# Kernel optimization log

Measured on AMD Instinct MI355X. Metric: run time of the kernel, lower is better.

The kernel has to match this reference:

```python
import jax, jax.numpy as jnp
import numpy as np
import math

D_MODEL = 1024
FFN = 4096
NUM_HEAD = 16
HEAD_DIM = 64
BATCH = 4
SEQ = 2048
EPS = 1e-5


def _lin(k, out_dim, in_dim):
    bound = 1.0 / math.sqrt(in_dim)
    k1, k2 = jax.random.split(k)
    W = jax.random.uniform(k1, (out_dim, in_dim), jnp.float32, -bound, bound)
    b = jax.random.uniform(k2, (out_dim,), jnp.float32, -bound, bound)
    return W, b


def setup_inputs() -> dict:
    key = jax.random.key(0)
    ks = jax.random.split(key, 12)
    x = jax.random.normal(ks[0], (BATCH, SEQ, D_MODEL), jnp.float32)
    mask = jnp.zeros((SEQ, SEQ), jnp.float32)  # additive mask, broadcast over [H,B,S,S]
    Wq, bq = _lin(ks[1], D_MODEL, D_MODEL)
    Wk, bk = _lin(ks[2], D_MODEL, D_MODEL)
    Wv, bv = _lin(ks[3], D_MODEL, D_MODEL)
    Wo, bo = _lin(ks[4], D_MODEL, D_MODEL)
    gamma = jnp.ones((D_MODEL,), jnp.float32)
    beta = jnp.zeros((D_MODEL,), jnp.float32)
    W1, b1 = _lin(ks[5], FFN, D_MODEL)
    W2, b2 = _lin(ks[6], FFN // 2, FFN)
    W3, b3 = _lin(ks[7], FFN // 4, FFN // 2)
    W4, b4 = _lin(ks[8], D_MODEL, FFN // 4)
    Wl, bl = _lin(ks[9], D_MODEL, D_MODEL)
    return dict(x=x, mask=mask, Wq=Wq, bq=bq, Wk=Wk, bk=bk, Wv=Wv, bv=bv,
                Wo=Wo, bo=bo, gamma=gamma, beta=beta,
                W1=W1, b1=b1, W2=W2, b2=b2, W3=W3, b3=b3, W4=W4, b4=b4,
                Wl=Wl, bl=bl)


def _layernorm(x, gamma, beta):
    mean = jnp.mean(x, axis=-1, keepdims=True)
    var = jnp.mean((x - mean) ** 2, axis=-1, keepdims=True)
    return gamma * ((x - mean) / jnp.sqrt(var + EPS)) + beta


def _attention(x, mask, Wq, bq, Wk, bk, Wv, bv, Wo, bo):
    B, S, _ = x.shape
    def heads(W, b):
        return (x @ W.T + b).reshape(B, S, NUM_HEAD, HEAD_DIM).transpose(0, 2, 1, 3)
    q, k, v = heads(Wq, bq), heads(Wk, bk), heads(Wv, bv)  # [B,H,S,D]
    scaled = jnp.einsum('bhsd,bhtd->bhst', q, k) / math.sqrt(HEAD_DIM)
    # faithful to source: permute to [H,B,S,S], add mask, softmax, NaN->0,
    # then sum over dim=1 (which is BATCH here) -> [H,S,S]
    scaled = scaled.transpose(1, 0, 2, 3) + mask
    attn = jax.nn.softmax(scaled, axis=-1)
    attn = jnp.where(jnp.isnan(attn), 0.0, attn)
    A = jnp.sum(attn, axis=1)  # [H,S,S]
    V = jnp.einsum('hst,bhtd->bhsd', A, v)  # broadcast matmul as in torch
    V = V.transpose(0, 2, 1, 3).reshape(B, S, NUM_HEAD * HEAD_DIM)
    return V @ Wo.T + bo


def _ffn(x, W1, b1, W2, b2, W3, b3, W4, b4):
    x = jax.nn.relu(x @ W1.T + b1)
    x = jax.nn.relu(x @ W2.T + b2)
    x = jax.nn.relu(x @ W3.T + b3)
    return x @ W4.T + b4


def reference(x, mask, Wq, bq, Wk, bk, Wv, bv, Wo, bo, gamma, beta,
              W1, b1, W2, b2, W3, b3, W4, b4, Wl, bl):
    res = x
    x = _attention(x, mask, Wq, bq, Wk, bk, Wv, bv, Wo, bo)
    x = _layernorm(x + res, gamma, beta)
    res = x
    x = _ffn(x, W1, b1, W2, b2, W3, b3, W4, b4)
    x = _layernorm(res + x, gamma, beta)
    return x @ Wl.T + bl
```

## Files before the change

### kernel.cpp

```cpp
#include <hip/hip_runtime.h>
#include <stdint.h>

#define SEQL 2048
#define DM 1024
#define NH 16
#define DHD 64
#define NB 4
#define MT 8192

typedef __attribute__((ext_vector_type(8))) short bf16x8;
typedef __attribute__((ext_vector_type(4))) float f32x4;

__device__ __forceinline__ unsigned short f2bf(float f) {
  uint32_t u = __builtin_bit_cast(uint32_t, f);
  return (unsigned short)((u + 0x7FFFu + ((u >> 16) & 1u)) >> 16);
}
__device__ __forceinline__ float bf2f(unsigned short h) {
  return __builtin_bit_cast(float, (uint32_t)h << 16);
}
__device__ __forceinline__ float fexp2(float x) {
  float r;
  asm volatile("v_exp_f32 %0, %1" : "=v"(r) : "v"(x));
  return r;
}
__device__ __forceinline__ void glds16(const void* g, void* l) {
  __builtin_amdgcn_global_load_lds(
      (const __attribute__((address_space(1))) void*)g,
      (__attribute__((address_space(3))) void*)l, 16, 0, 0);
}
__device__ __forceinline__ void bar() {
  asm volatile("" ::: "memory");
  __builtin_amdgcn_s_barrier();
  asm volatile("" ::: "memory");
}
__device__ __forceinline__ void vm4() { asm volatile("s_waitcnt vmcnt(4)" ::: "memory"); }
__device__ __forceinline__ void vm0() { asm volatile("s_waitcnt vmcnt(0)" ::: "memory"); }

__global__ __launch_bounds__(256) void cast_f32_bf16(
    const float* __restrict__ in, unsigned short* __restrict__ out, int n8) {
  int i = blockIdx.x * 256 + threadIdx.x;
  if (i >= n8) return;
  const float4* p = (const float4*)(in + (size_t)i * 8);
  float4 a = p[0], b = p[1];
  uint32_t w0 = f2bf(a.x) | ((uint32_t)f2bf(a.y) << 16);
  uint32_t w1 = f2bf(a.z) | ((uint32_t)f2bf(a.w) << 16);
  uint32_t w2 = f2bf(b.x) | ((uint32_t)f2bf(b.y) << 16);
  uint32_t w3 = f2bf(b.z) | ((uint32_t)f2bf(b.w) << 16);
  int4 v = {(int)w0, (int)w1, (int)w2, (int)w3};
  *(int4*)(out + (size_t)i * 8) = v;
}

__global__ __launch_bounds__(256) void addb(
    const unsigned short* __restrict__ a, unsigned short* __restrict__ bio, int n8) {
  int i = blockIdx.x * 256 + threadIdx.x;
  if (i >= n8) return;
  int4 va = *(const int4*)(a + (size_t)i * 8);
  int4 vb = *(const int4*)(bio + (size_t)i * 8);
  uint32_t* pa = (uint32_t*)&va;
  uint32_t* pb = (uint32_t*)&vb;
  int4 vo;
  uint32_t* po = (uint32_t*)&vo;
#pragma unroll
  for (int j = 0; j < 4; j++) {
    float lo = bf2f((unsigned short)pa[j]) + bf2f((unsigned short)pb[j]);
    float hi = bf2f((unsigned short)(pa[j] >> 16)) + bf2f((unsigned short)(pb[j] >> 16));
    po[j] = f2bf(lo) | ((uint32_t)f2bf(hi) << 16);
  }
  *(int4*)(bio + (size_t)i * 8) = vo;
}

__global__ __launch_bounds__(256) void vtrans(
    const unsigned short* __restrict__ V, unsigned short* __restrict__ Vt) {
  __shared__ unsigned short td[64][72];
  const int blk = blockIdx.x;
  const int t64 = blk & 31;
  const int b = (blk >> 5) & 3;
  const int h = blk >> 7;
  const int tid = threadIdx.x;
  const int r = tid >> 3, c8 = (tid & 7) * 8;
  const unsigned short* src = V + (size_t)(b * SEQL + t64 * 64) * DM + h * 64;
#pragma unroll
  for (int half = 0; half < 2; half++) {
    int4 v = *(const int4*)(src + (size_t)(r + half * 32) * DM + c8);
    *(int4*)&td[r + half * 32][c8] = v;
  }
  __syncthreads();
  unsigned short* dst = Vt + (size_t)((h * 4 + b) * 64) * SEQL + t64 * 64;
#pragma unroll
  for (int half = 0; half < 2; half++) {
    int tk = tid + half * 256;
    int d = tk >> 3, tc = (tk & 7) * 8;
    unsigned short tmp[8];
#pragma unroll
    for (int j = 0; j < 8; j++) tmp[j] = td[tc + j][d];
    *(int4*)(dst + (size_t)d * SEQL + tc) = *(int4*)tmp;
  }
}

template <int MS, int NS, int MR, int MH>
__device__ __forceinline__ void mmaQ(f32x4 (&acc)[MR][4],
                                     const bf16x8 (&Ar)[MH][2],
                                     const bf16x8 (&Br)[2][2]) {
  __builtin_amdgcn_s_setprio(1);
#pragma unroll
  for (int m = 0; m < MH; m++)
#pragma unroll
    for (int n = 0; n < 2; n++)
#pragma unroll
      for (int kk = 0; kk < 2; kk++)
        acc[MS * MH + m][NS * 2 + n] = __builtin_amdgcn_mfma_f32_16x16x32_bf16(
            Ar[m][kk], Br[n][kk], acc[MS * MH + m][NS * 2 + n], 0, 0, 0);
  __builtin_amdgcn_s_setprio(0);
}

template <int MH>
__device__ __forceinline__ void loadF(bf16x8 (&Ar)[MH][2], const char* base,
                                      int row0, int g) {
#pragma unroll
  for (int m = 0; m < MH; m++) {
    int row = row0 + m * 16;
    int sw = (row & 7) << 4;
    Ar[m][0] = *(const bf16x8*)(base + row * 128 + ((g << 4) ^ sw));
    Ar[m][1] = *(const bf16x8*)(base + row * 128 + (((4 + g) << 4) ^ sw));
  }
}

template <int BM, bool RELU, int OMODE>
__global__ __launch_bounds__(512, 2) void gemm8(
    const unsigned short* __restrict__ Ag, const unsigned short* __restrict__ Bg,
    const float* __restrict__ bias0, const float* __restrict__ bias1,
    const float* __restrict__ bias2, void* C0, void* C1, void* C2, int N, int K,
    float sc0) {
  constexpr int MR = BM / 32;
  constexpr int MH = MR / 2;
  constexpr int AT = BM * 128;
  constexpr int BT = 256 * 128;
  __shared__ __align__(16) char lds[2 * AT + 2 * BT];
  char* Ab0 = lds;
  char* Ab1 = lds + AT;
  char* Bb0 = lds + 2 * AT;
  char* Bb1 = lds + 2 * AT + BT;

  const int tid = threadIdx.x;
  const int wid = tid >> 6, lane = tid & 63;
  const int wr = wid >> 2, wc = wid & 3;
  const int g = lane >> 4, ln = lane & 15;

  const int nbx = N >> 8;
  const int nwg = gridDim.x;
  const int cpx = nwg >> 3;
  const int wg = (blockIdx.x & 7) * cpx + (blockIdx.x >> 3);
  const int bm = wg / nbx, bn = wg % nbx;

  f32x4 acc[MR][4];
#pragma unroll
  for (int m = 0; m < MR; m++)
#pragma unroll
    for (int n = 0; n < 4; n++) acc[m][n] = (f32x4){0.f, 0.f, 0.f, 0.f};

  const int srow = wid * 8 + (lane >> 3);
  const int cs8 = ((lane & 7) ^ (lane >> 3)) * 8;
  const unsigned short* aBase = Ag + (size_t)(bm * BM + srow) * K + cs8;
  const unsigned short* bBase = Bg + (size_t)(bn * 256 + srow) * K + cs8;
  const int wofs = wid * 1024;

  auto stageA = [&](char* buf, int tt, int h) {
    const unsigned short* src = aBase + (size_t)(h * (BM / 2)) * K + tt * 64;
    char* dst = buf + h * (AT / 2) + wofs;
    glds16(src, dst);
    if constexpr (BM == 256) glds16(src + (size_t)64 * K, dst + 8192);
  };
  auto stageB = [&](char* buf, int tt, int h) {
    const unsigned short* src = bBase + (size_t)(h * 128) * K + tt * 64;
    char* dst = buf + h * (BT / 2) + wofs;
    glds16(src, dst);
    glds16(src + (size_t)64 * K, dst + 8192);
  };

  const int np = K >> 7;
  const int rowA0 = wr * (BM / 2) + ln;
  const int rowB0 = wc * 64 + ln;

  stageA(Ab0, 0, 0);
  stageA(Ab0, 0, 1);
  stageB(Bb0, 0, 0);
  stageB(Bb0, 0, 1);
  stageB(Bb1, 1, 0);
  stageB(Bb1, 1, 1);
  vm4();
  bar();

  bf16x8 Ar[MH][2], Br0[2][2], Br1[2][2];
  for (int i = 0; i < np; i++) {
    const int t = 2 * i;
    const bool sg = (i + 1 < np);
    loadF<MH>(Ar, Ab0, rowA0, g);
    loadF<2>(Br0, Bb0, rowB0, g);
    stageA(Ab1, t + 1, 0);
    bar();
    mmaQ<0, 0>(acc, Ar, Br0);
    bar();
    loadF<2>(Br1, Bb0, rowB0 + 32, g);
    stageA(Ab1, t + 1, 1);
    bar();
    mmaQ<0, 1>(acc, Ar, Br1);
    bar();
    loadF<MH>(Ar, Ab0, rowA0 + MH * 16, g);
    if (sg) stageB(Bb0, t + 2, 0);
    bar();
    mmaQ<1, 1>(acc, Ar, Br1);
    bar();
    if (sg) stageB(Bb0, t + 2, 1);
    bar();
    mmaQ<1, 0>(acc, Ar, Br0);
    if (sg) vm4(); else vm0();
    bar();
    loadF<MH>(Ar, Ab1, rowA0, g);
    loadF<2>(Br0, Bb1, rowB0, g);
    if (sg) stageA(Ab0, t + 2, 0);
    bar();
    mmaQ<0, 0>(acc, Ar, Br0);
    bar();
    loadF<2>(Br1, Bb1, rowB0 + 32, g);
    if (sg) stageA(Ab0, t + 2, 1);
    bar();
    mmaQ<0, 1>(acc, Ar, Br1);
    bar();
    loadF<MH>(Ar, Ab1, rowA0 + MH * 16, g);
    if (sg) stageB(Bb1, t + 3, 0);
    bar();
    mmaQ<1, 1>(acc, Ar, Br1);
    bar();
    if (sg) stageB(Bb1, t + 3, 1);
    bar();
    mmaQ<1, 0>(acc, Ar, Br0);
    if (sg) vm4();
    bar();
  }

  const int c0 = bn * 256 + wc * 64;
  const float* bias = bias0;
  float scl = sc0;
  unsigned short* outb = (unsigned short*)C0;
  float* outf = (float*)C0;
  int ldC = N;
  if constexpr (OMODE == 2) {
    int seg = bn >> 2;
    bias = seg == 0 ? bias0 : (seg == 1 ? bias1 : bias2);
    outb = (unsigned short*)(seg == 0 ? C0 : (seg == 1 ? C1 : C2));
    scl = seg == 0 ? sc0 : 1.0f;
    ldC = 1024;
  }
#pragma unroll
  for (int am = 0; am < MR; am++) {
#pragma unroll
    for (int n = 0; n < 4; n++) {
      int col = c0 + n * 16 + ln;
      int colL = (OMODE == 2) ? (col & 1023) : col;
      float bv = bias[colL];
#pragma unroll
      for (int r = 0; r < 4; r++) {
        int row = bm * BM + wr * (BM / 2) + am * 16 + g * 4 + r;
        float v = (acc[am][n][r] + bv) * scl;
        if constexpr (RELU) v = fmaxf(v, 0.f);
        if constexpr (OMODE == 0)
          outf[(size_t)row * ldC + colL] = v;
        else
          outb[(size_t)row * ldC + colL] = f2bf(v);
      }
    }
  }
}

__global__ __launch_bounds__(256) void attn_stats(
    const unsigned short* __restrict__ Q, const unsigned short* __restrict__ Kb,
    float* __restrict__ lst) {
  __shared__ unsigned short sK[64 * 64];
  const int blk = blockIdx.x;
  const int sblk = blk & 31;
  const int bh = blk >> 5;
  const int b = bh >> 4, h = bh & 15;
  const int tid = threadIdx.x;
  const int wid = tid >> 6, lane = tid & 63;
  const int g = lane >> 4;
  const int s0 = sblk * 64 + wid * 16;

  const unsigned short* qp =
      Q + (size_t)(b * SEQL + s0 + (lane & 15)) * DM + h * DHD + g * 8;
  bf16x8 q0 = *(const bf16x8*)qp;
  bf16x8 q1 = *(const bf16x8*)(qp + 32);

  const int srow = tid >> 3;
  const int sch = (tid & 7) ^ (srow & 7);
  const unsigned short* kg =
      Kb + (size_t)(b * SEQL + srow) * DM + h * DHD + sch * 8;
  char* l0 = (char*)sK + wid * 1024;
  char* l1 = (char*)sK + 4096 + wid * 1024;

  float lsum = 0.f;
  for (int t0 = 0; t0 < SEQL; t0 += 64) {
    __syncthreads();
    glds16(kg + (size_t)t0 * DM, l0);
    glds16(kg + (size_t)(t0 + 32) * DM, l1);
    __syncthreads();
#pragma unroll
    for (int tt = 0; tt < 4; tt++) {
      int row = tt * 16 + (lane & 15);
      const char* base = (const char*)sK + row * 128;
      bf16x8 k0 = *(const bf16x8*)(base + ((g ^ (row & 7)) * 16));
      bf16x8 k1 = *(const bf16x8*)(base + (((g + 4) ^ (row & 7)) * 16));
      f32x4 sc = {0.f, 0.f, 0.f, 0.f};
      sc = __builtin_amdgcn_mfma_f32_16x16x32_bf16(k0, q0, sc, 0, 0, 0);
      sc = __builtin_amdgcn_mfma_f32_16x16x32_bf16(k1, q1, sc, 0, 0, 0);
      lsum += fexp2(sc[0]) + fexp2(sc[1]) + fexp2(sc[2]) + fexp2(sc[3]);
    }
  }
  lsum += __shfl_xor(lsum, 16);
  lsum += __shfl_xor(lsum, 32);
  if (lane < 16) lst[(size_t)bh * SEQL + s0 + lane] = lsum;
}

__global__ __launch_bounds__(256) void attn_apply(
    const unsigned short* __restrict__ Q, const unsigned short* __restrict__ Kb,
    const unsigned short* __restrict__ Vt, const float* __restrict__ lst,
    unsigned short* __restrict__ op0, unsigned short* __restrict__ op1) {
  __shared__ unsigned short sK[4][32 * 64];
  __shared__ unsigned short vT[4][64 * 32];
  __shared__ unsigned short a_lds[4][16][40];
  const int blk = blockIdx.x;
  const int tpart = blk & 1;
  const int sblk = (blk >> 1) & 31;
  const int h = blk >> 6;
  const int tid = threadIdx.x;
  const int wid = tid >> 6, lane = tid & 63;
  const int g = lane >> 4, ln = lane & 15;
  const int s0 = sblk * 64 + wid * 16;
  const int tbase = tpart * (SEQL / 2);

  bf16x8 q[4][2];
#pragma unroll
  for (int b = 0; b < 4; b++) {
    const unsigned short* qp =
        Q + (size_t)(b * SEQL + s0 + ln) * DM + h * DHD + g * 8;
    q[b][0] = *(const bf16x8*)qp;
    q[b][1] = *(const bf16x8*)(qp + 32);
  }
  float rl[4];
#pragma unroll
  for (int b = 0; b < 4; b++)
    rl[b] = 1.0f / lst[(size_t)(b * NH + h) * SEQL + s0 + ln];

  f32x4 o[4][4];
#pragma unroll
  for (int b = 0; b < 4; b++)
#pragma unroll
    for (int c = 0; c < 4; c++) o[b][c] = (f32x4){0.f, 0.f, 0.f, 0.f};

  const int krow = tid >> 3;
  const int kch = (tid & 7) ^ (krow & 7);
  const unsigned short* vsrc =
      Vt + (size_t)((h * 4 + wid) * 64 + (lane >> 2)) * SEQL + (lane & 3) * 8;

  for (int t0 = tbase; t0 < tbase + SEQL / 2; t0 += 32) {
    __syncthreads();
#pragma unroll
    for (int b = 0; b < 4; b++)
      glds16(Kb + (size_t)(b * SEQL + t0 + krow) * DM + h * DHD + kch * 8,
             (char*)sK + b * 4096 + wid * 1024);
#pragma unroll
    for (int qq = 0; qq < 4; qq++)
      glds16(vsrc + (size_t)(qq * 16) * SEQL + t0,
             (char*)vT + wid * 4096 + qq * 1024);
    __syncthreads();

    float at[2][4];
#pragma unroll
    for (int tt = 0; tt < 2; tt++)
#pragma unroll
      for (int r = 0; r < 4; r++) at[tt][r] = 0.f;
#pragma unroll
    for (int b = 0; b < 4; b++) {
#pragma unroll
      for (int tt = 0; tt < 2; tt++) {
        int row = tt * 16 + ln;
        const char* base = (const char*)sK + b * 4096 + row * 128;
        bf16x8 k0 = *(const bf16x8*)(base + ((g ^ (row & 7)) * 16));
        bf16x8 k1 = *(const bf16x8*)(base + (((g + 4) ^ (row & 7)) * 16));
        f32x4 sc = {0.f, 0.f, 0.f, 0.f};
        sc = __builtin_amdgcn_mfma_f32_16x16x32_bf16(k0, q[b][0], sc, 0, 0, 0);
        sc = __builtin_amdgcn_mfma_f32_16x16x32_bf16(k1, q[b][1], sc, 0, 0, 0);
#pragma unroll
        for (int r = 0; r < 4; r++)
          at[tt][r] = fmaf(fexp2(sc[r]), rl[b], at[tt][r]);
      }
    }
#pragma unroll
    for (int tt = 0; tt < 2; tt++)
#pragma unroll
      for (int r = 0; r < 4; r++)
        a_lds[wid][ln][tt * 16 + g * 4 + r] = f2bf(at[tt][r]);
    bf16x8 af = *(const bf16x8*)&a_lds[wid][ln][g * 8];
#pragma unroll
    for (int b = 0; b < 4; b++)
#pragma unroll
      for (int c = 0; c < 4; c++) {
        bf16x8 bv =
            *(const bf16x8*)((const char*)vT + b * 4096 + (c * 16 + ln) * 64 + g * 16);
        o[b][c] = __builtin_amdgcn_mfma_f32_16x16x32_bf16(af, bv, o[b][c], 0, 0, 0);
      }
  }

  unsigned short* op = tpart ? op1 : op0;
#pragma unroll
  for (int b = 0; b < 4; b++)
#pragma unroll
    for (int c = 0; c < 4; c++)
#pragma unroll
      for (int r = 0; r < 4; r++) {
        int srow = s0 + g * 4 + r;
        size_t off = (size_t)(b * SEQL + srow) * DM + h * DHD + c * 16 + ln;
        op[off] = f2bf(o[b][c][r]);
      }
}

template <bool RESBF16>
__global__ __launch_bounds__(256) void ln_kernel(
    const float* __restrict__ a, const void* __restrict__ res,
    const float* __restrict__ gamma, const float* __restrict__ beta,
    unsigned short* __restrict__ obf) {
  __shared__ float red[8];
  const int row = blockIdx.x;
  const int tid = threadIdx.x;
  const size_t base = (size_t)row * DM + tid * 4;
  float4 va = *(const float4*)(a + base);
  float v0, v1, v2, v3;
  if (RESBF16) {
    const unsigned short* rp = (const unsigned short*)res + base;
    ushort4 u = *(const ushort4*)rp;
    v0 = va.x + bf2f(u.x);
    v1 = va.y + bf2f(u.y);
    v2 = va.z + bf2f(u.z);
    v3 = va.w + bf2f(u.w);
  } else {
    float4 vr = *(const float4*)((const float*)res + base);
    v0 = va.x + vr.x;
    v1 = va.y + vr.y;
    v2 = va.z + vr.z;
    v3 = va.w + vr.w;
  }
  float sum = v0 + v1 + v2 + v3;
#pragma unroll
  for (int off = 1; off < 64; off <<= 1) sum += __shfl_xor(sum, off);
  const int wid = tid >> 6, lane = tid & 63;
  if (lane == 0) red[wid] = sum;
  __syncthreads();
  float mean = (red[0] + red[1] + red[2] + red[3]) * (1.0f / DM);
  float d0 = v0 - mean, d1 = v1 - mean, d2 = v2 - mean, d3 = v3 - mean;
  float sq = d0 * d0 + d1 * d1 + d2 * d2 + d3 * d3;
#pragma unroll
  for (int off = 1; off < 64; off <<= 1) sq += __shfl_xor(sq, off);
  if (lane == 0) red[4 + wid] = sq;
  __syncthreads();
  float var = (red[4] + red[5] + red[6] + red[7]) * (1.0f / DM);
  float rstd = rsqrtf(var + 1e-5f);
  float4 gm = *(const float4*)(gamma + tid * 4);
  float4 bb = *(const float4*)(beta + tid * 4);
  float o0 = gm.x * (d0 * rstd) + bb.x;
  float o1 = gm.y * (d1 * rstd) + bb.y;
  float o2 = gm.z * (d2 * rstd) + bb.z;
  float o3 = gm.w * (d3 * rstd) + bb.w;
  uint32_t w0 = f2bf(o0) | ((uint32_t)f2bf(o1) << 16);
  uint32_t w1 = f2bf(o2) | ((uint32_t)f2bf(o3) << 16);
  uint2 pk = {w0, w1};
  *(uint2*)(obf + base) = pk;
}

extern "C" void kernel_launch(void* const* d_in, const int* in_sizes, int n_in,
                              void* d_out, int out_size, void* d_ws, size_t ws_size,
                              hipStream_t stream) {
  (void)in_sizes; (void)n_in; (void)out_size; (void)ws_size;
  const float* x  = (const float*)d_in[0];
  const float* Wq = (const float*)d_in[2];  const float* bq = (const float*)d_in[3];
  const float* Wk = (const float*)d_in[4];  const float* bk = (const float*)d_in[5];
  const float* Wv = (const float*)d_in[6];  const float* bv = (const float*)d_in[7];
  const float* Wo = (const float*)d_in[8];  const float* bo = (const float*)d_in[9];
  const float* gamma = (const float*)d_in[10]; const float* beta = (const float*)d_in[11];
  const float* W1 = (const float*)d_in[12]; const float* b1 = (const float*)d_in[13];
  const float* W2 = (const float*)d_in[14]; const float* b2 = (const float*)d_in[15];
  const float* W3 = (const float*)d_in[16]; const float* b3 = (const float*)d_in[17];
  const float* W4 = (const float*)d_in[18]; const float* b4 = (const float*)d_in[19];
  const float* Wl = (const float*)d_in[20]; const float* bl = (const float*)d_in[21];
  float* out = (float*)d_out;

  char* w = (char*)d_ws;
  const size_t MB = 1024 * 1024;
  unsigned short* xb   = (unsigned short*)(w);
  unsigned short* Qb   = (unsigned short*)(w + 16 * MB);
  unsigned short* Kbf  = (unsigned short*)(w + 32 * MB);
  unsigned short* Vbf  = (unsigned short*)(w + 48 * MB);
  float* lst = (float*)(w + 64 * MB);
  unsigned short* ctx  = (unsigned short*)(w + 65 * MB);
  unsigned short* wbuf = (unsigned short*)(w + 81 * MB);
  float* aproj = (float*)(w + 97 * MB);
  unsigned short* ln1b = (unsigned short*)(w + 129 * MB);
  unsigned short* Vt   = (unsigned short*)(w + 97 * MB);
  unsigned short* op0  = (unsigned short*)(w);
  unsigned short* op1  = ctx;
  unsigned short* h1   = (unsigned short*)(w);
  unsigned short* h2   = (unsigned short*)(w + 97 * MB);
  unsigned short* h3   = (unsigned short*)(w + 65 * MB);
  float* ffo  = (float*)(w);
  unsigned short* ln2b = (unsigned short*)(w + 32 * MB);

  auto cast = [&](const float* src, unsigned short* dst, size_t n) {
    int n8 = (int)(n / 8);
    cast_f32_bf16<<<dim3((n8 + 255) / 256), dim3(256), 0, stream>>>(src, dst, n8);
  };
  const float QSCALE = 0.125f * 1.44269504088896f;

  cast(x, xb, (size_t)MT * DM);
  cast(Wq, wbuf, (size_t)DM * DM);
  cast(Wk, wbuf + (size_t)DM * DM, (size_t)DM * DM);
  cast(Wv, wbuf + (size_t)2 * DM * DM, (size_t)DM * DM);
  gemm8<256, false, 2><<<dim3((MT / 256) * (3072 / 256)), dim3(512), 0, stream>>>(
      xb, wbuf, bq, bk, bv, Qb, Kbf, Vbf, 3072, 1024, QSCALE);
  vtrans<<<dim3(NH * NB * (SEQL / 64)), dim3(256), 0, stream>>>(Vbf, Vt);
  attn_stats<<<dim3(NB * NH * (SEQL / 64)), dim3(256), 0, stream>>>(Qb, Kbf, lst);
  attn_apply<<<dim3(NH * 32 * 2), dim3(256), 0, stream>>>(Qb, Kbf, Vt, lst, op0, op1);
  addb<<<dim3((MT * DM / 8 + 255) / 256), dim3(256), 0, stream>>>(op0, ctx, MT * DM / 8);
  cast(Wo, wbuf, (size_t)DM * DM);
  gemm8<128, false, 0><<<dim3((MT / 128) * 4), dim3(512), 0, stream>>>(
      ctx, wbuf, bo, nullptr, nullptr, aproj, nullptr, nullptr, 1024, 1024, 1.0f);
  ln_kernel<false><<<dim3(MT), dim3(256), 0, stream>>>(aproj, x, gamma, beta, ln1b);
  cast(W1, wbuf, (size_t)4096 * DM);
  gemm8<256, true, 1><<<dim3((MT / 256) * 16), dim3(512), 0, stream>>>(
      ln1b, wbuf, b1, nullptr, nullptr, h1, nullptr, nullptr, 4096, 1024, 1.0f);
  cast(W2, wbuf, (size_t)2048 * 4096);
  gemm8<256, true, 1><<<dim3((MT / 256) * 8), dim3(512), 0, stream>>>(
      h1, wbuf, b2, nullptr, nullptr, h2, nullptr, nullptr, 2048, 4096, 1.0f);
  cast(W3, wbuf, (size_t)1024 * 2048);
  gemm8<128, true, 1><<<dim3((MT / 128) * 4), dim3(512), 0, stream>>>(
      h2, wbuf, b3, nullptr, nullptr, h3, nullptr, nullptr, 1024, 2048, 1.0f);
  cast(W4, wbuf, (size_t)DM * DM);
  gemm8<128, false, 0><<<dim3((MT / 128) * 4), dim3(512), 0, stream>>>(
      h3, wbuf, b4, nullptr, nullptr, ffo, nullptr, nullptr, 1024, 1024, 1.0f);
  ln_kernel<true><<<dim3(MT), dim3(256), 0, stream>>>(ffo, ln1b, gamma, beta, ln2b);
  cast(Wl, wbuf, (size_t)DM * DM);
  gemm8<128, false, 0><<<dim3((MT / 128) * 4), dim3(512), 0, stream>>>(
      ln2b, wbuf, bl, nullptr, nullptr, out, nullptr, nullptr, 1024, 1024, 1.0f);
}
```

Baseline: 652.4 us.

## Permute V transpose so attention probabilities feed MFMA directly from registers

The V transpose kernel now writes each 32-token group in a permuted order that matches the MFMA accumulator layout of the score tiles. The apply kernel can then pack its probabilities straight into a bf16 A-operand with v_cvt_pk_bf16_f32 instead of round-tripping them through an LDS scratch buffer. V tiles in LDS are also XOR-swizzled to reduce bank conflicts. This removes per-iteration LDS writes and reads and the scalar bf16 conversions, but relies on a delicate layout contract between vtrans and attn_apply.

After: 636.4 us. 2.4% less time.

```diff
diff --git a/kernel.cpp b/kernel.cpp
--- a/kernel.cpp
+++ b/kernel.cpp
@@ -21,6 +21,11 @@
 __device__ __forceinline__ float fexp2(float x) {
   float r;
   asm volatile("v_exp_f32 %0, %1" : "=v"(r) : "v"(x));
+  return r;
+}
+__device__ __forceinline__ uint32_t cvtpk(float lo, float hi) {
+  uint32_t r;
+  asm volatile("v_cvt_pk_bf16_f32 %0, %1, %2" : "=v"(r) : "v"(lo), "v"(hi));
   return r;
 }
 __device__ __forceinline__ void glds16(const void* g, void* l) {
@@ -90,9 +95,12 @@
   for (int half = 0; half < 2; half++) {
     int tk = tid + half * 256;
     int d = tk >> 3, tc = (tk & 7) * 8;
+    int gq = (tc >> 3) & 3;
+    int b32 = tc & 32;
     unsigned short tmp[8];
 #pragma unroll
-    for (int j = 0; j < 8; j++) tmp[j] = td[tc + j][d];
+    for (int j = 0; j < 8; j++)
+      tmp[j] = td[b32 + gq * 4 + (j & 3) + 16 * (j >> 2)][d];
     *(int4*)(dst + (size_t)d * SEQL + tc) = *(int4*)tmp;
   }
 }
@@ -322,11 +330,10 @@
 
 __global__ __launch_bounds__(256) void attn_apply(
     const unsigned short* __restrict__ Q, const unsigned short* __restrict__ Kb,
-    const unsigned short* __restrict__ Vt, const float* __restrict__ lst,
+    const unsigned short* __restrict__ Vtp, const float* __restrict__ lst,
     unsigned short* __restrict__ op0, unsigned short* __restrict__ op1) {
   __shared__ unsigned short sK[4][32 * 64];
-  __shared__ unsigned short vT[4][64 * 32];
-  __shared__ unsigned short a_lds[4][16][40];
+  __shared__ unsigned short sV[4][64 * 32];
   const int blk = blockIdx.x;
   const int tpart = blk & 1;
   const int sblk = (blk >> 1) & 31;
@@ -358,8 +365,11 @@
 
   const int krow = tid >> 3;
   const int kch = (tid & 7) ^ (krow & 7);
-  const unsigned short* vsrc =
-      Vt + (size_t)((h * 4 + wid) * 64 + (lane >> 2)) * SEQL + (lane & 3) * 8;
+  const int vrow = wid * 16 + (lane >> 2);
+  const int vch = (lane & 3) ^ ((vrow >> 1) & 3);
+  const unsigned short* vbase =
+      Vtp + (size_t)(h * 256 + vrow) * SEQL + vch * 8;
+  const int vswz = (ln >> 1) & 3;
 
   for (int t0 = tbase; t0 < tbase + SEQL / 2; t0 += 32) {
     __syncthreads();
@@ -368,9 +378,9 @@
       glds16(Kb + (size_t)(b * SEQL + t0 + krow) * DM + h * DHD + kch * 8,
              (char*)sK + b * 4096 + wid * 1024);
 #pragma unroll
-    for (int qq = 0; qq < 4; qq++)
-      glds16(vsrc + (size_t)(qq * 16) * SEQL + t0,
-             (char*)vT + wid * 4096 + qq * 1024);
+    for (int b = 0; b < 4; b++)
+      glds16(vbase + (size_t)(b * 64) * SEQL + t0,
+             (char*)sV + b * 4096 + wid * 1024);
     __syncthreads();
 
     float at[2][4];
@@ -394,20 +404,24 @@
           at[tt][r] = fmaf(fexp2(sc[r]), rl[b], at[tt][r]);
       }
     }
-#pragma unroll
-    for (int tt = 0; tt < 2; tt++)
-#pragma unroll
-      for (int r = 0; r < 4; r++)
-        a_lds[wid][ln][tt * 16 + g * 4 + r] = f2bf(at[tt][r]);
-    bf16x8 af = *(const bf16x8*)&a_lds[wid][ln][g * 8];
-#pragma unroll
-    for (int b = 0; b < 4; b++)
+    uint32_t aw0 = cvtpk(at[0][0], at[0][1]);
+    uint32_t aw1 = cvtpk(at[0][2], at[0][3]);
+    uint32_t aw2 = cvtpk(at[1][0], at[1][1]);
+    uint32_t aw3 = cvtpk(at[1][2], at[1][3]);
+    int4 awv = {(int)aw0, (int)aw1, (int)aw2, (int)aw3};
+    bf16x8 apk = __builtin_bit_cast(bf16x8, awv);
+
+#pragma unroll
+    for (int b = 0; b < 4; b++) {
 #pragma unroll
       for (int c = 0; c < 4; c++) {
-        bf16x8 bv =
-            *(const bf16x8*)((const char*)vT + b * 4096 + (c * 16 + ln) * 64 + g * 16);
-        o[b][c] = __builtin_amdgcn_mfma_f32_16x16x32_bf16(af, bv, o[b][c], 0, 0, 0);
+        int row = c * 16 + ln;
+        const char* vb =
+            (const char*)sV + b * 4096 + row * 64 + (((g ^ vswz)) << 4);
+        bf16x8 vf = *(const bf16x8*)vb;
+        o[b][c] = __builtin_amdgcn_mfma_f32_16x16x32_bf16(apk, vf, o[b][c], 0, 0, 0);
       }
+    }
   }
 
   unsigned short* op = tpart ? op1 : op0;
@@ -505,7 +519,6 @@
   unsigned short* ln1b = (unsigned short*)(w + 129 * MB);
   unsigned short* Vt   = (unsigned short*)(w + 97 * MB);
   unsigned short* op0  = (unsigned short*)(w);
-  unsigned short* op1  = ctx;
   unsigned short* h1   = (unsigned short*)(w);
   unsigned short* h2   = (unsigned short*)(w + 97 * MB);
   unsigned short* h3   = (unsigned short*)(w + 65 * MB);
@@ -526,7 +539,7 @@
       xb, wbuf, bq, bk, bv, Qb, Kbf, Vbf, 3072, 1024, QSCALE);
   vtrans<<<dim3(NH * NB * (SEQL / 64)), dim3(256), 0, stream>>>(Vbf, Vt);
   attn_stats<<<dim3(NB * NH * (SEQL / 64)), dim3(256), 0, stream>>>(Qb, Kbf, lst);
-  attn_apply<<<dim3(NH * 32 * 2), dim3(256), 0, stream>>>(Qb, Kbf, Vt, lst, op0, op1);
+  attn_apply<<<dim3(NH * 32 * 2), dim3(256), 0, stream>>>(Qb, Kbf, Vt, lst, op0, ctx);
   addb<<<dim3((MT * DM / 8 + 255) / 256), dim3(256), 0, stream>>>(op0, ctx, MT * DM / 8);
   cast(Wo, wbuf, (size_t)DM * DM);
   gemm8<128, false, 0><<<dim3((MT / 128) * 4), dim3(512), 0, stream>>>(
```
